# Kernel optimization log

Measured on AMD Instinct MI355X. Metric: run time of the kernel, lower is better.

## Reference

```python
import jax, jax.numpy as jnp
import numpy as np

B, Q, K, D, H = 16, 256, 256, 256, 256


def setup_inputs() -> dict:
    key = jax.random.key(0)
    ks = jax.random.split(key, 7)
    queries = jax.random.normal(ks[0], (B, Q, D), dtype=jnp.float32)
    keys = jax.random.normal(ks[1], (B, K, D), dtype=jnp.float32)
    values = jax.random.normal(ks[2], (B, K, D), dtype=jnp.float32)
    valid_lens = jax.random.randint(ks[3], (B,), 1, K + 1).astype(jnp.int64)
    # LazyLinear weights, no bias: W_q: D->H, W_k: D->H, w_v: H->1
    s = 1.0 / np.sqrt(D)
    Wq = jax.random.uniform(ks[4], (D, H), jnp.float32, -s, s)
    Wk = jax.random.uniform(ks[5], (D, H), jnp.float32, -s, s)
    sv = 1.0 / np.sqrt(H)
    wv = jax.random.uniform(ks[6], (H,), jnp.float32, -sv, sv)
    return {"queries": queries, "keys": keys, "values": values,
            "valid_lens": valid_lens, "Wq": Wq, "Wk": Wk, "wv": wv}


def reference(queries, keys, values, valid_lens, Wq, Wk, wv):
    q = queries @ Wq                      # [B,Q,H]
    k = keys @ Wk                         # [B,K,H]
    feats = jnp.tanh(q[:, :, None, :] + k[:, None, :, :])  # [B,Q,K,H]
    scores = jnp.einsum('bqkh,h->bqk', feats, wv)           # [B,Q,K]
    mask = jnp.arange(scores.shape[-1]) < valid_lens[:, None, None]  # [B,1,K]
    attn = jax.nn.softmax(jnp.where(mask, scores, -1e6), axis=-1)
    return jnp.einsum('bqk,bkv->bqv', attn, values)
```

## Files before the change

kernel.cpp:

```cpp
#include <hip/hip_runtime.h>

#define B_ 16
#define QN 256
#define KN 256
#define DN 256
#define HN 256

#define LOG2E 1.4426950408889634f
#define TWOLOG2E 2.8853900817779268f

__device__ inline float readlane_f(float v, int l) {
    return __uint_as_float(__builtin_amdgcn_readlane(__float_as_uint(v), l));
}

__global__ __launch_bounds__(256) void proj_kernel(const float* __restrict__ Xq,
                                                   const float* __restrict__ Xk,
                                                   const float* __restrict__ Wq,
                                                   const float* __restrict__ Wk,
                                                   float* __restrict__ EQ,
                                                   float* __restrict__ EKT,
                                                   float scale) {
    const int nb = (int)gridDim.x >> 1;
    int blk = blockIdx.x;
    const bool is_q = blk < nb;
    const float* X;
    const float* W;
    if (is_q) { X = Xq; W = Wq; }
    else      { X = Xk; W = Wk; blk -= nb; }
    const int row0 = blk * 16;

    __shared__ float xl[16][260];
    __shared__ float trans[16][260];
    const int tid = threadIdx.x;

    {
        const float4* src = (const float4*)(X + (size_t)row0 * DN);
#pragma unroll
        for (int i = 0; i < 4; ++i) {
            int idx = tid + 256 * i;
            int r = idx >> 6, c = (idx & 63) << 2;
            *(float4*)&xl[r][c] = src[idx];
        }
    }
    __syncthreads();

    const int rg = tid >> 6;
    const int h4 = (tid & 63) << 2;

    float4 acc[4];
#pragma unroll
    for (int r = 0; r < 4; ++r) acc[r] = make_float4(0.f, 0.f, 0.f, 0.f);

    float4 wb0[4], wb1[4];
#pragma unroll
    for (int j = 0; j < 4; ++j) wb0[j] = *(const float4*)&W[(size_t)j * HN + h4];

#define PROJ_COMP(WB, D0)                                                      \
    do {                                                                       \
        float4 x[4];                                                           \
        _Pragma("unroll") for (int r = 0; r < 4; ++r)                          \
            x[r] = *(const float4*)&xl[(rg << 2) + r][(D0)];                   \
        _Pragma("unroll") for (int r = 0; r < 4; ++r) {                        \
            acc[r].x = fmaf(x[r].x, WB[0].x, acc[r].x);                        \
            acc[r].y = fmaf(x[r].x, WB[0].y, acc[r].y);                        \
            acc[r].z = fmaf(x[r].x, WB[0].z, acc[r].z);                        \
            acc[r].w = fmaf(x[r].x, WB[0].w, acc[r].w);                        \
            acc[r].x = fmaf(x[r].y, WB[1].x, acc[r].x);                        \
            acc[r].y = fmaf(x[r].y, WB[1].y, acc[r].y);                        \
            acc[r].z = fmaf(x[r].y, WB[1].z, acc[r].z);                        \
            acc[r].w = fmaf(x[r].y, WB[1].w, acc[r].w);                        \
            acc[r].x = fmaf(x[r].z, WB[2].x, acc[r].x);                        \
            acc[r].y = fmaf(x[r].z, WB[2].y, acc[r].y);                        \
            acc[r].z = fmaf(x[r].z, WB[2].z, acc[r].z);                        \
            acc[r].w = fmaf(x[r].z, WB[2].w, acc[r].w);                        \
            acc[r].x = fmaf(x[r].w, WB[3].x, acc[r].x);                        \
            acc[r].y = fmaf(x[r].w, WB[3].y, acc[r].y);                        \
            acc[r].z = fmaf(x[r].w, WB[3].z, acc[r].z);                        \
            acc[r].w = fmaf(x[r].w, WB[3].w, acc[r].w);                        \
        }                                                                      \
    } while (0)

    for (int d0 = 0; d0 < DN; d0 += 8) {
#pragma unroll
        for (int j = 0; j < 4; ++j)
            wb1[j] = *(const float4*)&W[(size_t)(d0 + 4 + j) * HN + h4];
        PROJ_COMP(wb0, d0);
        if (d0 + 8 < DN) {
#pragma unroll
            for (int j = 0; j < 4; ++j)
                wb0[j] = *(const float4*)&W[(size_t)(d0 + 8 + j) * HN + h4];
        }
        PROJ_COMP(wb1, d0 + 4);
    }

#pragma unroll
    for (int r = 0; r < 4; ++r) {
        acc[r].x = __builtin_amdgcn_exp2f(acc[r].x * scale);
        acc[r].y = __builtin_amdgcn_exp2f(acc[r].y * scale);
        acc[r].z = __builtin_amdgcn_exp2f(acc[r].z * scale);
        acc[r].w = __builtin_amdgcn_exp2f(acc[r].w * scale);
    }

    if (is_q) {
#pragma unroll
        for (int r = 0; r < 4; ++r)
            *(float4*)&EQ[(size_t)(row0 + (rg << 2) + r) * HN + h4] = acc[r];
    } else {
#pragma unroll
        for (int r = 0; r < 4; ++r)
            *(float4*)&trans[(rg << 2) + r][h4] = acc[r];
        __syncthreads();
        const int b = row0 >> 8, kloc0 = row0 & 255;
        float* dstb = EKT + (size_t)b * 32 * 256 * 8;
#pragma unroll
        for (int i = 0; i < 4; ++i) {
            int idx = i * 256 + tid;
            int u4 = (idx & 1) << 2;
            int kj = (idx >> 1) & 15;
            int h0 = idx >> 5;
            float4 val = *(const float4*)&trans[kj][h0 * 8 + u4];
            *(float4*)&dstb[((size_t)h0 * 256 + kloc0 + kj) * 8 + u4] = val;
        }
    }
}

__global__ __launch_bounds__(256, 4) void attn_kernel(const float* __restrict__ EQ,
                                                      const float* __restrict__ EKT,
                                                      const float* __restrict__ wv,
                                                      const int* __restrict__ lens,
                                                      const float* __restrict__ V,
                                                      float* __restrict__ OUT) {
    const int b = blockIdx.y;
    const int q0 = blockIdx.x * 4;
    const int len = lens[b];

    __shared__ float eq_lds[4][256];
    __shared__ float wv_lds[256];
    __shared__ float part[4][4][256];
    __shared__ float maxb[4][4];
    __shared__ float sumb[4][4];

    const int tid = threadIdx.x;
    const int w = tid >> 6, lane = tid & 63;

    {
        int r = tid >> 6, c4 = (tid & 63) << 2;
        *(float4*)&eq_lds[r][c4] =
            *(const float4*)&EQ[((size_t)b * QN + q0 + r) * HN + c4];
        if (tid < 64) *(float4*)&wv_lds[tid << 2] = *(const float4*)&wv[tid << 2];
    }
    __syncthreads();

    const bool act = (w * 64) < len;
    float acc[4] = {0.f, 0.f, 0.f, 0.f};

#define WINDOW(KA, KB, H8)                                                        \
    do {                                                                          \
        float4 wa = *(const float4*)&wv_lds[(H8)];                                \
        float4 wb = *(const float4*)&wv_lds[(H8) + 4];                            \
        _Pragma("unroll") for (int qq = 0; qq < 4; ++qq) {                        \
            float4 qa = *(const float4*)&eq_lds[qq][(H8)];                        \
            float4 qb = *(const float4*)&eq_lds[qq][(H8) + 4];                    \
            float t = acc[qq];                                                    \
            t = fmaf(wa.x, __builtin_amdgcn_rcpf(fmaf(qa.x, KA.x, 1.f)), t);      \
            t = fmaf(wa.y, __builtin_amdgcn_rcpf(fmaf(qa.y, KA.y, 1.f)), t);      \
            t = fmaf(wa.z, __builtin_amdgcn_rcpf(fmaf(qa.z, KA.z, 1.f)), t);      \
            t = fmaf(wa.w, __builtin_amdgcn_rcpf(fmaf(qa.w, KA.w, 1.f)), t);      \
            t = fmaf(wb.x, __builtin_amdgcn_rcpf(fmaf(qb.x, KB.x, 1.f)), t);      \
            t = fmaf(wb.y, __builtin_amdgcn_rcpf(fmaf(qb.y, KB.y, 1.f)), t);      \
            t = fmaf(wb.z, __builtin_amdgcn_rcpf(fmaf(qb.z, KB.z, 1.f)), t);      \
            t = fmaf(wb.w, __builtin_amdgcn_rcpf(fmaf(qb.w, KB.w, 1.f)), t);      \
            acc[qq] = t;                                                          \
        }                                                                         \
    } while (0)

    if (act) {
        const float* kp = EKT + (size_t)b * (32 * 256 * 8) + (size_t)(w * 64 + lane) * 8;
        float4 ka0 = *(const float4*)&kp[0];
        float4 kb0 = *(const float4*)&kp[4];
        float4 ka1, kb1;
        for (int hw = 0; hw < 32; hw += 2) {
            const float* kp1 = kp + (size_t)(hw + 1) * 2048;
            ka1 = *(const float4*)&kp1[0];
            kb1 = *(const float4*)&kp1[4];
            WINDOW(ka0, kb0, hw * 8);
            if (hw + 2 < 32) {
                const float* kp2 = kp + (size_t)(hw + 2) * 2048;
                ka0 = *(const float4*)&kp2[0];
                kb0 = *(const float4*)&kp2[4];
            }
            WINDOW(ka1, kb1, hw * 8 + 8);
        }
    }

    const bool kvalid = (w * 64 + lane) < len;
    float xs0 = kvalid ? (-2.f * acc[0]) : -1e6f;
    float xs1 = kvalid ? (-2.f * acc[1]) : -1e6f;
    float xs2 = kvalid ? (-2.f * acc[2]) : -1e6f;
    float xs3 = kvalid ? (-2.f * acc[3]) : -1e6f;

    float m0 = xs0, m1 = xs1, m2 = xs2, m3 = xs3;
#pragma unroll
    for (int off = 32; off; off >>= 1) {
        m0 = fmaxf(m0, __shfl_xor(m0, off, 64));
        m1 = fmaxf(m1, __shfl_xor(m1, off, 64));
        m2 = fmaxf(m2, __shfl_xor(m2, off, 64));
        m3 = fmaxf(m3, __shfl_xor(m3, off, 64));
    }
    if (lane == 0) {
        maxb[w][0] = m0; maxb[w][1] = m1; maxb[w][2] = m2; maxb[w][3] = m3;
    }
    __syncthreads();
    float g0 = fmaxf(fmaxf(maxb[0][0], maxb[1][0]), fmaxf(maxb[2][0], maxb[3][0]));
    float g1 = fmaxf(fmaxf(maxb[0][1], maxb[1][1]), fmaxf(maxb[2][1], maxb[3][1]));
    float g2 = fmaxf(fmaxf(maxb[0][2], maxb[1][2]), fmaxf(maxb[2][2], maxb[3][2]));
    float g3 = fmaxf(fmaxf(maxb[0][3], maxb[1][3]), fmaxf(maxb[2][3], maxb[3][3]));

    float p0 = __builtin_amdgcn_exp2f((xs0 - g0) * LOG2E);
    float p1 = __builtin_amdgcn_exp2f((xs1 - g1) * LOG2E);
    float p2 = __builtin_amdgcn_exp2f((xs2 - g2) * LOG2E);
    float p3 = __builtin_amdgcn_exp2f((xs3 - g3) * LOG2E);

    float s0 = p0, s1 = p1, s2 = p2, s3 = p3;
#pragma unroll
    for (int off = 32; off; off >>= 1) {
        s0 += __shfl_xor(s0, off, 64);
        s1 += __shfl_xor(s1, off, 64);
        s2 += __shfl_xor(s2, off, 64);
        s3 += __shfl_xor(s3, off, 64);
    }
    if (lane == 0) {
        sumb[w][0] = s0; sumb[w][1] = s1; sumb[w][2] = s2; sumb[w][3] = s3;
    }
    __syncthreads();
    float t0 = (sumb[0][0] + sumb[1][0]) + (sumb[2][0] + sumb[3][0]);
    float t1 = (sumb[0][1] + sumb[1][1]) + (sumb[2][1] + sumb[3][1]);
    float t2 = (sumb[0][2] + sumb[1][2]) + (sumb[2][2] + sumb[3][2]);
    float t3 = (sumb[0][3] + sumb[1][3]) + (sumb[2][3] + sumb[3][3]);
    p0 *= 1.f / t0;
    p1 *= 1.f / t1;
    p2 *= 1.f / t2;
    p3 *= 1.f / t3;

    float4 op0 = make_float4(0.f, 0.f, 0.f, 0.f);
    float4 op1 = op0, op2 = op0, op3 = op0;
    if (act) {
        int kmax = len - w * 64;
        if (kmax > 64) kmax = 64;
        const float* vb = V + ((size_t)b * KN + (size_t)w * 64) * DN + (lane << 2);

#define PV_STEP(KK, VV)                                                        \
    do {                                                                       \
        float b0 = readlane_f(p0, (KK));                                       \
        float b1 = readlane_f(p1, (KK));                                       \
        float b2 = readlane_f(p2, (KK));                                       \
        float b3 = readlane_f(p3, (KK));                                       \
        op0.x = fmaf(b0, VV.x, op0.x); op0.y = fmaf(b0, VV.y, op0.y);          \
        op0.z = fmaf(b0, VV.z, op0.z); op0.w = fmaf(b0, VV.w, op0.w);          \
        op1.x = fmaf(b1, VV.x, op1.x); op1.y = fmaf(b1, VV.y, op1.y);          \
        op1.z = fmaf(b1, VV.z, op1.z); op1.w = fmaf(b1, VV.w, op1.w);          \
        op2.x = fmaf(b2, VV.x, op2.x); op2.y = fmaf(b2, VV.y, op2.y);          \
        op2.z = fmaf(b2, VV.z, op2.z); op2.w = fmaf(b2, VV.w, op2.w);          \
        op3.x = fmaf(b3, VV.x, op3.x); op3.y = fmaf(b3, VV.y, op3.y);          \
        op3.z = fmaf(b3, VV.z, op3.z); op3.w = fmaf(b3, VV.w, op3.w);          \
    } while (0)

        int kk = 0;
        for (; kk + 4 <= kmax; kk += 4) {
            float4 v0 = *(const float4*)&vb[(size_t)(kk + 0) * DN];
            float4 v1 = *(const float4*)&vb[(size_t)(kk + 1) * DN];
            float4 v2 = *(const float4*)&vb[(size_t)(kk + 2) * DN];
            float4 v3 = *(const float4*)&vb[(size_t)(kk + 3) * DN];
            PV_STEP(kk + 0, v0);
            PV_STEP(kk + 1, v1);
            PV_STEP(kk + 2, v2);
            PV_STEP(kk + 3, v3);
        }
        for (; kk < kmax; ++kk) {
            float4 v0 = *(const float4*)&vb[(size_t)kk * DN];
            PV_STEP(kk, v0);
        }
    }
    {
        const int d4 = lane << 2;
        *(float4*)&part[w][0][d4] = op0;
        *(float4*)&part[w][1][d4] = op1;
        *(float4*)&part[w][2][d4] = op2;
        *(float4*)&part[w][3][d4] = op3;
    }
    __syncthreads();

    {
        const int q = tid >> 6, ln = tid & 63;
        const int d4 = ln << 2;
        float4 r0 = *(const float4*)&part[0][q][d4];
        float4 r1 = *(const float4*)&part[1][q][d4];
        float4 r2 = *(const float4*)&part[2][q][d4];
        float4 r3 = *(const float4*)&part[3][q][d4];
        float4 r = make_float4((r0.x + r1.x) + (r2.x + r3.x),
                               (r0.y + r1.y) + (r2.y + r3.y),
                               (r0.z + r1.z) + (r2.z + r3.z),
                               (r0.w + r1.w) + (r2.w + r3.w));
        *(float4*)&OUT[((size_t)b * QN + q0 + q) * DN + d4] = r;
    }
}

extern "C" void kernel_launch(void* const* d_in, const int* in_sizes, int n_in,
                              void* d_out, int out_size, void* d_ws, size_t ws_size,
                              hipStream_t stream) {
    const float* queries = (const float*)d_in[0];
    const float* keys    = (const float*)d_in[1];
    const float* values  = (const float*)d_in[2];
    const int*   lens    = (const int*)d_in[3];
    const float* Wq      = (const float*)d_in[4];
    const float* Wk      = (const float*)d_in[5];
    const float* wv      = (const float*)d_in[6];
    float* out = (float*)d_out;

    float* eq  = (float*)d_ws;
    float* ekT = eq + (size_t)B_ * QN * HN;

    proj_kernel<<<(B_ * QN + B_ * KN) / 16, 256, 0, stream>>>(
        queries, keys, Wq, Wk, eq, ekT, TWOLOG2E);

    dim3 gB(QN / 4, B_);
    attn_kernel<<<gB, 256, 0, stream>>>(eq, ekT, wv, lens, values, out);
}
```

Measured before the change: 58.59 us.

## Process eight queries per block and interleave batches across the 1D grid

Each attention block now handles 8 queries instead of 4, so every EKT key load from global memory is reused across twice as many queries and V rows are read half as often. The grid becomes 1D with the batch index in the low bits, which spreads batches with different valid lengths across neighbouring blocks and should balance load better. In exchange, per-thread register use (8 accumulators, 8 float4 outputs) and LDS use roughly double. The grid also halves to 512 blocks, which could reduce occupancy or cause spills under the launch bounds of 4.

```diff
diff --git a/kernel.cpp b/kernel.cpp
--- a/kernel.cpp
+++ b/kernel.cpp
@@ -130,35 +130,36 @@
                                                       const int* __restrict__ lens,
                                                       const float* __restrict__ V,
                                                       float* __restrict__ OUT) {
-    const int b = blockIdx.y;
-    const int q0 = blockIdx.x * 4;
+    const int b = blockIdx.x & 15;
+    const int q0 = (blockIdx.x >> 4) * 8;
     const int len = lens[b];
 
-    __shared__ float eq_lds[4][256];
+    __shared__ float eq_lds[8][256];
     __shared__ float wv_lds[256];
-    __shared__ float part[4][4][256];
-    __shared__ float maxb[4][4];
-    __shared__ float sumb[4][4];
+    __shared__ float part[4][8][256];
+    __shared__ float maxb[4][8];
+    __shared__ float sumb[4][8];
 
     const int tid = threadIdx.x;
     const int w = tid >> 6, lane = tid & 63;
 
     {
-        int r = tid >> 6, c4 = (tid & 63) << 2;
-        *(float4*)&eq_lds[r][c4] =
-            *(const float4*)&EQ[((size_t)b * QN + q0 + r) * HN + c4];
+        const float4* src = (const float4*)&EQ[((size_t)b * QN + q0) * HN];
+        float4* dst = (float4*)&eq_lds[0][0];
+        dst[tid] = src[tid];
+        dst[tid + 256] = src[tid + 256];
         if (tid < 64) *(float4*)&wv_lds[tid << 2] = *(const float4*)&wv[tid << 2];
     }
     __syncthreads();
 
     const bool act = (w * 64) < len;
-    float acc[4] = {0.f, 0.f, 0.f, 0.f};
+    float acc[8] = {0.f, 0.f, 0.f, 0.f, 0.f, 0.f, 0.f, 0.f};
 
 #define WINDOW(KA, KB, H8)                                                        \
     do {                                                                          \
         float4 wa = *(const float4*)&wv_lds[(H8)];                                \
         float4 wb = *(const float4*)&wv_lds[(H8) + 4];                            \
-        _Pragma("unroll") for (int qq = 0; qq < 4; ++qq) {                        \
+        _Pragma("unroll") for (int qq = 0; qq < 8; ++qq) {                        \
             float4 qa = *(const float4*)&eq_lds[qq][(H8)];                        \
             float4 qb = *(const float4*)&eq_lds[qq][(H8) + 4];                    \
             float t = acc[qq];                                                    \
@@ -194,56 +195,38 @@
     }
 
     const bool kvalid = (w * 64 + lane) < len;
-    float xs0 = kvalid ? (-2.f * acc[0]) : -1e6f;
-    float xs1 = kvalid ? (-2.f * acc[1]) : -1e6f;
-    float xs2 = kvalid ? (-2.f * acc[2]) : -1e6f;
-    float xs3 = kvalid ? (-2.f * acc[3]) : -1e6f;
-
-    float m0 = xs0, m1 = xs1, m2 = xs2, m3 = xs3;
-#pragma unroll
-    for (int off = 32; off; off >>= 1) {
-        m0 = fmaxf(m0, __shfl_xor(m0, off, 64));
-        m1 = fmaxf(m1, __shfl_xor(m1, off, 64));
-        m2 = fmaxf(m2, __shfl_xor(m2, off, 64));
-        m3 = fmaxf(m3, __shfl_xor(m3, off, 64));
-    }
-    if (lane == 0) {
-        maxb[w][0] = m0; maxb[w][1] = m1; maxb[w][2] = m2; maxb[w][3] = m3;
-    }
-    __syncthreads();
-    float g0 = fmaxf(fmaxf(maxb[0][0], maxb[1][0]), fmaxf(maxb[2][0], maxb[3][0]));
-    float g1 = fmaxf(fmaxf(maxb[0][1], maxb[1][1]), fmaxf(maxb[2][1], maxb[3][1]));
-    float g2 = fmaxf(fmaxf(maxb[0][2], maxb[1][2]), fmaxf(maxb[2][2], maxb[3][2]));
-    float g3 = fmaxf(fmaxf(maxb[0][3], maxb[1][3]), fmaxf(maxb[2][3], maxb[3][3]));
-
-    float p0 = __builtin_amdgcn_exp2f((xs0 - g0) * LOG2E);
-    float p1 = __builtin_amdgcn_exp2f((xs1 - g1) * LOG2E);
-    float p2 = __builtin_amdgcn_exp2f((xs2 - g2) * LOG2E);
-    float p3 = __builtin_amdgcn_exp2f((xs3 - g3) * LOG2E);
-
-    float s0 = p0, s1 = p1, s2 = p2, s3 = p3;
-#pragma unroll
-    for (int off = 32; off; off >>= 1) {
-        s0 += __shfl_xor(s0, off, 64);
-        s1 += __shfl_xor(s1, off, 64);
-        s2 += __shfl_xor(s2, off, 64);
-        s3 += __shfl_xor(s3, off, 64);
-    }
-    if (lane == 0) {
-        sumb[w][0] = s0; sumb[w][1] = s1; sumb[w][2] = s2; sumb[w][3] = s3;
-    }
-    __syncthreads();
-    float t0 = (sumb[0][0] + sumb[1][0]) + (sumb[2][0] + sumb[3][0]);
-    float t1 = (sumb[0][1] + sumb[1][1]) + (sumb[2][1] + sumb[3][1]);
-    float t2 = (sumb[0][2] + sumb[1][2]) + (sumb[2][2] + sumb[3][2]);
-    float t3 = (sumb[0][3] + sumb[1][3]) + (sumb[2][3] + sumb[3][3]);
-    p0 *= 1.f / t0;
-    p1 *= 1.f / t1;
-    p2 *= 1.f / t2;
-    p3 *= 1.f / t3;
-
-    float4 op0 = make_float4(0.f, 0.f, 0.f, 0.f);
-    float4 op1 = op0, op2 = op0, op3 = op0;
+    float p[8];
+#pragma unroll
+    for (int qq = 0; qq < 8; ++qq) {
+        float x = kvalid ? (-2.f * acc[qq]) : -1e6f;
+        acc[qq] = x;
+        float mm = x;
+#pragma unroll
+        for (int off = 32; off; off >>= 1) mm = fmaxf(mm, __shfl_xor(mm, off, 64));
+        if (lane == 0) maxb[w][qq] = mm;
+    }
+    __syncthreads();
+#pragma unroll
+    for (int qq = 0; qq < 8; ++qq) {
+        float g = fmaxf(fmaxf(maxb[0][qq], maxb[1][qq]),
+                        fmaxf(maxb[2][qq], maxb[3][qq]));
+        float pp = __builtin_amdgcn_exp2f((acc[qq] - g) * LOG2E);
+        p[qq] = pp;
+        float ss = pp;
+#pragma unroll
+        for (int off = 32; off; off >>= 1) ss += __shfl_xor(ss, off, 64);
+        if (lane == 0) sumb[w][qq] = ss;
+    }
+    __syncthreads();
+#pragma unroll
+    for (int qq = 0; qq < 8; ++qq) {
+        float t = (sumb[0][qq] + sumb[1][qq]) + (sumb[2][qq] + sumb[3][qq]);
+        p[qq] *= 1.f / t;
+    }
+
+    float4 op[8];
+#pragma unroll
+    for (int qq = 0; qq < 8; ++qq) op[qq] = make_float4(0.f, 0.f, 0.f, 0.f);
     if (act) {
         int kmax = len - w * 64;
         if (kmax > 64) kmax = 64;
@@ -251,18 +234,13 @@
 
 #define PV_STEP(KK, VV)                                                        \
     do {                                                                       \
-        float b0 = readlane_f(p0, (KK));                                       \
-        float b1 = readlane_f(p1, (KK));                                       \
-        float b2 = readlane_f(p2, (KK));                                       \
-        float b3 = readlane_f(p3, (KK));                                       \
-        op0.x = fmaf(b0, VV.x, op0.x); op0.y = fmaf(b0, VV.y, op0.y);          \
-        op0.z = fmaf(b0, VV.z, op0.z); op0.w = fmaf(b0, VV.w, op0.w);          \
-        op1.x = fmaf(b1, VV.x, op1.x); op1.y = fmaf(b1, VV.y, op1.y);          \
-        op1.z = fmaf(b1, VV.z, op1.z); op1.w = fmaf(b1, VV.w, op1.w);          \
-        op2.x = fmaf(b2, VV.x, op2.x); op2.y = fmaf(b2, VV.y, op2.y);          \
-        op2.z = fmaf(b2, VV.z, op2.z); op2.w = fmaf(b2, VV.w, op2.w);          \
-        op3.x = fmaf(b3, VV.x, op3.x); op3.y = fmaf(b3, VV.y, op3.y);          \
-        op3.z = fmaf(b3, VV.z, op3.z); op3.w = fmaf(b3, VV.w, op3.w);          \
+        _Pragma("unroll") for (int qq = 0; qq < 8; ++qq) {                     \
+            float bp = readlane_f(p[qq], (KK));                                \
+            op[qq].x = fmaf(bp, VV.x, op[qq].x);                               \
+            op[qq].y = fmaf(bp, VV.y, op[qq].y);                               \
+            op[qq].z = fmaf(bp, VV.z, op[qq].z);                               \
+            op[qq].w = fmaf(bp, VV.w, op[qq].w);                               \
+        }                                                                      \
     } while (0)
 
         int kk = 0;
@@ -283,25 +261,27 @@
     }
     {
         const int d4 = lane << 2;
-        *(float4*)&part[w][0][d4] = op0;
-        *(float4*)&part[w][1][d4] = op1;
-        *(float4*)&part[w][2][d4] = op2;
-        *(float4*)&part[w][3][d4] = op3;
+#pragma unroll
+        for (int qq = 0; qq < 8; ++qq) *(float4*)&part[w][qq][d4] = op[qq];
     }
     __syncthreads();
 
     {
-        const int q = tid >> 6, ln = tid & 63;
+        const int ln = tid & 63;
         const int d4 = ln << 2;
-        float4 r0 = *(const float4*)&part[0][q][d4];
-        float4 r1 = *(const float4*)&part[1][q][d4];
-        float4 r2 = *(const float4*)&part[2][q][d4];
-        float4 r3 = *(const float4*)&part[3][q][d4];
-        float4 r = make_float4((r0.x + r1.x) + (r2.x + r3.x),
-                               (r0.y + r1.y) + (r2.y + r3.y),
-                               (r0.z + r1.z) + (r2.z + r3.z),
-                               (r0.w + r1.w) + (r2.w + r3.w));
-        *(float4*)&OUT[((size_t)b * QN + q0 + q) * DN + d4] = r;
+#pragma unroll
+        for (int half = 0; half < 2; ++half) {
+            const int q = (tid >> 6) + half * 4;
+            float4 r0 = *(const float4*)&part[0][q][d4];
+            float4 r1 = *(const float4*)&part[1][q][d4];
+            float4 r2 = *(const float4*)&part[2][q][d4];
+            float4 r3 = *(const float4*)&part[3][q][d4];
+            float4 r = make_float4((r0.x + r1.x) + (r2.x + r3.x),
+                                   (r0.y + r1.y) + (r2.y + r3.y),
+                                   (r0.z + r1.z) + (r2.z + r3.z),
+                                   (r0.w + r1.w) + (r2.w + r3.w));
+            *(float4*)&OUT[((size_t)b * QN + q0 + q) * DN + d4] = r;
+        }
     }
 }
 
@@ -323,6 +303,5 @@
     proj_kernel<<<(B_ * QN + B_ * KN) / 16, 256, 0, stream>>>(
         queries, keys, Wq, Wk, eq, ekT, TWOLOG2E);
 
-    dim3 gB(QN / 4, B_);
-    attn_kernel<<<gB, 256, 0, stream>>>(eq, ekT, wv, lens, values, out);
+    attn_kernel<<<(QN / 8) * B_, 256, 0, stream>>>(eq, ekT, wv, lens, values, out);
 }
```

New measurement: 69.22 us. 1.18x slower.

## Halve queries per attention block and retile projection to 8 rows x 2 cols

Applied to the files above, without the earlier changes.

The attention kernel now handles 2 queries per block instead of 4, which doubles the grid to 128x16 blocks and raises the occupancy hint to 8. This gives more parallelism and lower register pressure, at the cost of reloading each EK tile and V rows twice as often. The projection kernel is retiled so each thread computes 8 rows by 2 columns with double-buffered LDS and W loads, and it gets a launch bound of 2 waves. Together these aim to improve latency hiding, with the tradeoff of more redundant global traffic.

```diff
diff --git a/kernel.cpp b/kernel.cpp
--- a/kernel.cpp
+++ b/kernel.cpp
@@ -13,13 +13,13 @@
     return __uint_as_float(__builtin_amdgcn_readlane(__float_as_uint(v), l));
 }
 
-__global__ __launch_bounds__(256) void proj_kernel(const float* __restrict__ Xq,
-                                                   const float* __restrict__ Xk,
-                                                   const float* __restrict__ Wq,
-                                                   const float* __restrict__ Wk,
-                                                   float* __restrict__ EQ,
-                                                   float* __restrict__ EKT,
-                                                   float scale) {
+__global__ __launch_bounds__(256, 2) void proj_kernel(const float* __restrict__ Xq,
+                                                      const float* __restrict__ Xk,
+                                                      const float* __restrict__ Wq,
+                                                      const float* __restrict__ Wk,
+                                                      float* __restrict__ EQ,
+                                                      float* __restrict__ EKT,
+                                                      float scale) {
     const int nb = (int)gridDim.x >> 1;
     int blk = blockIdx.x;
     const bool is_q = blk < nb;
@@ -44,71 +44,69 @@
     }
     __syncthreads();
 
-    const int rg = tid >> 6;
-    const int h4 = (tid & 63) << 2;
-
-    float4 acc[4];
-#pragma unroll
-    for (int r = 0; r < 4; ++r) acc[r] = make_float4(0.f, 0.f, 0.f, 0.f);
-
-    float4 wb0[4], wb1[4];
-#pragma unroll
-    for (int j = 0; j < 4; ++j) wb0[j] = *(const float4*)&W[(size_t)j * HN + h4];
-
-#define PROJ_COMP(WB, D0)                                                      \
+    const int wvid = tid >> 6;
+    const int rbase = (wvid >> 1) << 3;
+    const int h2 = ((wvid & 1) << 7) | ((tid & 63) << 1);
+
+    float2 acc[8];
+#pragma unroll
+    for (int r = 0; r < 8; ++r) acc[r] = make_float2(0.f, 0.f);
+
+#define LOADW2(WS, D0)                                                         \
     do {                                                                       \
-        float4 x[4];                                                           \
-        _Pragma("unroll") for (int r = 0; r < 4; ++r)                          \
-            x[r] = *(const float4*)&xl[(rg << 2) + r][(D0)];                   \
-        _Pragma("unroll") for (int r = 0; r < 4; ++r) {                        \
-            acc[r].x = fmaf(x[r].x, WB[0].x, acc[r].x);                        \
-            acc[r].y = fmaf(x[r].x, WB[0].y, acc[r].y);                        \
-            acc[r].z = fmaf(x[r].x, WB[0].z, acc[r].z);                        \
-            acc[r].w = fmaf(x[r].x, WB[0].w, acc[r].w);                        \
-            acc[r].x = fmaf(x[r].y, WB[1].x, acc[r].x);                        \
-            acc[r].y = fmaf(x[r].y, WB[1].y, acc[r].y);                        \
-            acc[r].z = fmaf(x[r].y, WB[1].z, acc[r].z);                        \
-            acc[r].w = fmaf(x[r].y, WB[1].w, acc[r].w);                        \
-            acc[r].x = fmaf(x[r].z, WB[2].x, acc[r].x);                        \
-            acc[r].y = fmaf(x[r].z, WB[2].y, acc[r].y);                        \
-            acc[r].z = fmaf(x[r].z, WB[2].z, acc[r].z);                        \
-            acc[r].w = fmaf(x[r].z, WB[2].w, acc[r].w);                        \
-            acc[r].x = fmaf(x[r].w, WB[3].x, acc[r].x);                        \
-            acc[r].y = fmaf(x[r].w, WB[3].y, acc[r].y);                        \
-            acc[r].z = fmaf(x[r].w, WB[3].z, acc[r].z);                        \
-            acc[r].w = fmaf(x[r].w, WB[3].w, acc[r].w);                        \
+        _Pragma("unroll") for (int j = 0; j < 4; ++j)                          \
+            WS[j] = *(const float2*)&W[(size_t)((D0) + j) * HN + h2];          \
+    } while (0)
+
+#define LOADX8(XS, D0)                                                         \
+    do {                                                                       \
+        _Pragma("unroll") for (int r = 0; r < 8; ++r)                          \
+            XS[r] = *(const float4*)&xl[rbase + r][(D0)];                      \
+    } while (0)
+
+#define COMP2(WS, XS)                                                          \
+    do {                                                                       \
+        _Pragma("unroll") for (int r = 0; r < 8; ++r) {                        \
+            acc[r].x = fmaf(XS[r].x, WS[0].x, acc[r].x);                       \
+            acc[r].y = fmaf(XS[r].x, WS[0].y, acc[r].y);                       \
+            acc[r].x = fmaf(XS[r].y, WS[1].x, acc[r].x);                       \
+            acc[r].y = fmaf(XS[r].y, WS[1].y, acc[r].y);                       \
+            acc[r].x = fmaf(XS[r].z, WS[2].x, acc[r].x);                       \
+            acc[r].y = fmaf(XS[r].z, WS[2].y, acc[r].y);                       \
+            acc[r].x = fmaf(XS[r].w, WS[3].x, acc[r].x);                       \
+            acc[r].y = fmaf(XS[r].w, WS[3].y, acc[r].y);                       \
         }                                                                      \
     } while (0)
 
-    for (int d0 = 0; d0 < DN; d0 += 8) {
-#pragma unroll
-        for (int j = 0; j < 4; ++j)
-            wb1[j] = *(const float4*)&W[(size_t)(d0 + 4 + j) * HN + h4];
-        PROJ_COMP(wb0, d0);
-        if (d0 + 8 < DN) {
-#pragma unroll
-            for (int j = 0; j < 4; ++j)
-                wb0[j] = *(const float4*)&W[(size_t)(d0 + 8 + j) * HN + h4];
-        }
-        PROJ_COMP(wb1, d0 + 4);
-    }
-
-#pragma unroll
-    for (int r = 0; r < 4; ++r) {
+    {
+        float2 w0[4], w1[4];
+        float4 xA[8], xB[8];
+        LOADX8(xA, 0);
+        LOADX8(xB, 4);
+        LOADW2(w0, 0);
+        LOADW2(w1, 4);
+        for (int d0 = 0; d0 < DN - 8; d0 += 8) {
+            COMP2(w0, xA); LOADX8(xA, d0 + 8);  LOADW2(w0, d0 + 8);
+            COMP2(w1, xB); LOADX8(xB, d0 + 12); LOADW2(w1, d0 + 12);
+        }
+        COMP2(w0, xA);
+        COMP2(w1, xB);
+    }
+
+#pragma unroll
+    for (int r = 0; r < 8; ++r) {
         acc[r].x = __builtin_amdgcn_exp2f(acc[r].x * scale);
         acc[r].y = __builtin_amdgcn_exp2f(acc[r].y * scale);
-        acc[r].z = __builtin_amdgcn_exp2f(acc[r].z * scale);
-        acc[r].w = __builtin_amdgcn_exp2f(acc[r].w * scale);
     }
 
     if (is_q) {
 #pragma unroll
-        for (int r = 0; r < 4; ++r)
-            *(float4*)&EQ[(size_t)(row0 + (rg << 2) + r) * HN + h4] = acc[r];
+        for (int r = 0; r < 8; ++r)
+            *(float2*)&EQ[(size_t)(row0 + rbase + r) * HN + h2] = acc[r];
     } else {
 #pragma unroll
-        for (int r = 0; r < 4; ++r)
-            *(float4*)&trans[(rg << 2) + r][h4] = acc[r];
+        for (int r = 0; r < 8; ++r)
+            *(float2*)&trans[rbase + r][h2] = acc[r];
         __syncthreads();
         const int b = row0 >> 8, kloc0 = row0 & 255;
         float* dstb = EKT + (size_t)b * 32 * 256 * 8;
@@ -124,41 +122,41 @@
     }
 }
 
-__global__ __launch_bounds__(256, 4) void attn_kernel(const float* __restrict__ EQ,
+__global__ __launch_bounds__(256, 8) void attn_kernel(const float* __restrict__ EQ,
                                                       const float* __restrict__ EKT,
                                                       const float* __restrict__ wv,
                                                       const int* __restrict__ lens,
                                                       const float* __restrict__ V,
                                                       float* __restrict__ OUT) {
     const int b = blockIdx.y;
-    const int q0 = blockIdx.x * 4;
+    const int q0 = blockIdx.x * 2;
     const int len = lens[b];
 
-    __shared__ float eq_lds[4][256];
+    __shared__ float eq_lds[2][256];
     __shared__ float wv_lds[256];
-    __shared__ float part[4][4][256];
-    __shared__ float maxb[4][4];
-    __shared__ float sumb[4][4];
+    __shared__ float part[4][2][256];
+    __shared__ float maxb[4][2];
+    __shared__ float sumb[4][2];
 
     const int tid = threadIdx.x;
     const int w = tid >> 6, lane = tid & 63;
 
     {
-        int r = tid >> 6, c4 = (tid & 63) << 2;
-        *(float4*)&eq_lds[r][c4] =
-            *(const float4*)&EQ[((size_t)b * QN + q0 + r) * HN + c4];
-        if (tid < 64) *(float4*)&wv_lds[tid << 2] = *(const float4*)&wv[tid << 2];
+        const float4* src = (const float4*)&EQ[((size_t)b * QN + q0) * HN];
+        if (tid < 128) ((float4*)&eq_lds[0][0])[tid] = src[tid];
+        if (tid >= 192) *(float4*)&wv_lds[(tid - 192) << 2] =
+            ((const float4*)wv)[tid - 192];
     }
     __syncthreads();
 
     const bool act = (w * 64) < len;
-    float acc[4] = {0.f, 0.f, 0.f, 0.f};
+    float acc[2] = {0.f, 0.f};
 
 #define WINDOW(KA, KB, H8)                                                        \
     do {                                                                          \
         float4 wa = *(const float4*)&wv_lds[(H8)];                                \
         float4 wb = *(const float4*)&wv_lds[(H8) + 4];                            \
-        _Pragma("unroll") for (int qq = 0; qq < 4; ++qq) {                        \
+        _Pragma("unroll") for (int qq = 0; qq < 2; ++qq) {                        \
             float4 qa = *(const float4*)&eq_lds[qq][(H8)];                        \
             float4 qb = *(const float4*)&eq_lds[qq][(H8) + 4];                    \
             float t = acc[qq];                                                    \
@@ -196,54 +194,36 @@
     const bool kvalid = (w * 64 + lane) < len;
     float xs0 = kvalid ? (-2.f * acc[0]) : -1e6f;
     float xs1 = kvalid ? (-2.f * acc[1]) : -1e6f;
-    float xs2 = kvalid ? (-2.f * acc[2]) : -1e6f;
-    float xs3 = kvalid ? (-2.f * acc[3]) : -1e6f;
-
-    float m0 = xs0, m1 = xs1, m2 = xs2, m3 = xs3;
+
+    float m0 = xs0, m1 = xs1;
 #pragma unroll
     for (int off = 32; off; off >>= 1) {
         m0 = fmaxf(m0, __shfl_xor(m0, off, 64));
         m1 = fmaxf(m1, __shfl_xor(m1, off, 64));
-        m2 = fmaxf(m2, __shfl_xor(m2, off, 64));
-        m3 = fmaxf(m3, __shfl_xor(m3, off, 64));
-    }
-    if (lane == 0) {
-        maxb[w][0] = m0; maxb[w][1] = m1; maxb[w][2] = m2; maxb[w][3] = m3;
-    }
+    }
+    if (lane == 0) { maxb[w][0] = m0; maxb[w][1] = m1; }
     __syncthreads();
     float g0 = fmaxf(fmaxf(maxb[0][0], maxb[1][0]), fmaxf(maxb[2][0], maxb[3][0]));
     float g1 = fmaxf(fmaxf(maxb[0][1], maxb[1][1]), fmaxf(maxb[2][1], maxb[3][1]));
-    float g2 = fmaxf(fmaxf(maxb[0][2], maxb[1][2]), fmaxf(maxb[2][2], maxb[3][2]));
-    float g3 = fmaxf(fmaxf(maxb[0][3], maxb[1][3]), fmaxf(maxb[2][3], maxb[3][3]));
 
     float p0 = __builtin_amdgcn_exp2f((xs0 - g0) * LOG2E);
     float p1 = __builtin_amdgcn_exp2f((xs1 - g1) * LOG2E);
-    float p2 = __builtin_amdgcn_exp2f((xs2 - g2) * LOG2E);
-    float p3 = __builtin_amdgcn_exp2f((xs3 - g3) * LOG2E);
-
-    float s0 = p0, s1 = p1, s2 = p2, s3 = p3;
+
+    float s0 = p0, s1 = p1;
 #pragma unroll
     for (int off = 32; off; off >>= 1) {
         s0 += __shfl_xor(s0, off, 64);
         s1 += __shfl_xor(s1, off, 64);
-        s2 += __shfl_xor(s2, off, 64);
-        s3 += __shfl_xor(s3, off, 64);
-    }
-    if (lane == 0) {
-        sumb[w][0] = s0; sumb[w][1] = s1; sumb[w][2] = s2; sumb[w][3] = s3;
-    }
+    }
+    if (lane == 0) { sumb[w][0] = s0; sumb[w][1] = s1; }
     __syncthreads();
     float t0 = (sumb[0][0] + sumb[1][0]) + (sumb[2][0] + sumb[3][0]);
     float t1 = (sumb[0][1] + sumb[1][1]) + (sumb[2][1] + sumb[3][1]);
-    float t2 = (sumb[0][2] + sumb[1][2]) + (sumb[2][2] + sumb[3][2]);
-    float t3 = (sumb[0][3] + sumb[1][3]) + (sumb[2][3] + sumb[3][3]);
     p0 *= 1.f / t0;
     p1 *= 1.f / t1;
-    p2 *= 1.f / t2;
-    p3 *= 1.f / t3;
 
     float4 op0 = make_float4(0.f, 0.f, 0.f, 0.f);
-    float4 op1 = op0, op2 = op0, op3 = op0;
+    float4 op1 = op0;
     if (act) {
         int kmax = len - w * 64;
         if (kmax > 64) kmax = 64;
@@ -253,16 +233,10 @@
     do {                                                                       \
         float b0 = readlane_f(p0, (KK));                                       \
         float b1 = readlane_f(p1, (KK));                                       \
-        float b2 = readlane_f(p2, (KK));                                       \
-        float b3 = readlane_f(p3, (KK));                                       \
         op0.x = fmaf(b0, VV.x, op0.x); op0.y = fmaf(b0, VV.y, op0.y);          \
         op0.z = fmaf(b0, VV.z, op0.z); op0.w = fmaf(b0, VV.w, op0.w);          \
         op1.x = fmaf(b1, VV.x, op1.x); op1.y = fmaf(b1, VV.y, op1.y);          \
         op1.z = fmaf(b1, VV.z, op1.z); op1.w = fmaf(b1, VV.w, op1.w);          \
-        op2.x = fmaf(b2, VV.x, op2.x); op2.y = fmaf(b2, VV.y, op2.y);          \
-        op2.z = fmaf(b2, VV.z, op2.z); op2.w = fmaf(b2, VV.w, op2.w);          \
-        op3.x = fmaf(b3, VV.x, op3.x); op3.y = fmaf(b3, VV.y, op3.y);          \
-        op3.z = fmaf(b3, VV.z, op3.z); op3.w = fmaf(b3, VV.w, op3.w);          \
     } while (0)
 
         int kk = 0;
@@ -285,12 +259,10 @@
         const int d4 = lane << 2;
         *(float4*)&part[w][0][d4] = op0;
         *(float4*)&part[w][1][d4] = op1;
-        *(float4*)&part[w][2][d4] = op2;
-        *(float4*)&part[w][3][d4] = op3;
-    }
-    __syncthreads();
-
-    {
+    }
+    __syncthreads();
+
+    if (tid < 128) {
         const int q = tid >> 6, ln = tid & 63;
         const int d4 = ln << 2;
         float4 r0 = *(const float4*)&part[0][q][d4];
@@ -323,6 +295,6 @@
     proj_kernel<<<(B_ * QN + B_ * KN) / 16, 256, 0, stream>>>(
         queries, keys, Wq, Wk, eq, ekT, TWOLOG2E);
 
-    dim3 gB(QN / 4, B_);
+    dim3 gB(QN / 2, B_);
     attn_kernel<<<gB, 256, 0, stream>>>(eq, ekT, wv, lens, values, out);
 }
```

Result: faster. 56.28 us (-3.9%).
